# Performance work log

Hardware: AMD Instinct MI355X
Metric: run time of the kernel (lower is better)

## Reference

```python
import jax, jax.numpy as jnp
import numpy as np

B, S, N, DIN, DOUT = 8, 2048, 16, 1024, 1024

def setup_inputs() -> dict:
    key = jax.random.key(0)
    k1, k2, k3, k4 = jax.random.split(key, 4)
    x = jax.random.normal(k1, (B, S, DIN), dtype=jnp.float32)
    # selection_probs: per-batch mixture weights over total_options (rows sum to 1)
    logits = jax.random.uniform(k2, (B, N), dtype=jnp.float32)
    selection_probs = jax.nn.softmax(logits, axis=-1)
    # kaiming_uniform(a=sqrt(5)) over fan_in=DIN -> bound = 1/sqrt(DIN)
    bound = 1.0 / np.sqrt(DIN)
    weight = jax.random.uniform(k3, (N, DOUT, DIN), dtype=jnp.float32, minval=-bound, maxval=bound)
    bias = jax.random.uniform(k4, (N, DOUT), dtype=jnp.float32, minval=-bound, maxval=bound)
    return {"x": x, "selection_probs": selection_probs, "weight": weight, "bias": bias}

def reference(x, selection_probs, weight, bias):
    # Math identical to: einsum('nij,baj->bani', W, x) then einsum('bani,bn->bai', ., p)
    # but mixes weights per-batch first (same contraction, avoids the [B,S,N,DOUT] tensor).
    mixed_w = jnp.einsum('bn,nij->bij', selection_probs, weight)   # [B, DOUT, DIN]
    out = jnp.einsum('bij,baj->bai', mixed_w, x)                   # [B, S, DOUT]
    mixed_b = jnp.einsum('bn,ni->bi', selection_probs, bias)       # [B, DOUT]
    return out + mixed_b[:, None, :]
```

## Files before the change

### kernel.cpp

```cpp
#include <hip/hip_runtime.h>
#include <hip/hip_bf16.h>
#include <stdint.h>

#define BB 8
#define SS 2048
#define NEXP 16
#define DIN 1024
#define DOUT 1024

typedef short bf16x8 __attribute__((ext_vector_type(8)));
typedef float floatx4 __attribute__((ext_vector_type(4)));

__device__ __forceinline__ unsigned short f2bf(float f) {
    union { float f; unsigned int u; } v; v.f = f;
    unsigned int u = v.u;
    unsigned int r = u + 0x7FFFu + ((u >> 16) & 1u);
    return (unsigned short)(r >> 16);
}

__device__ __forceinline__ void gload16(const void* g, void* l) {
    __builtin_amdgcn_global_load_lds(
        (const __attribute__((address_space(1))) void*)g,
        (__attribute__((address_space(3))) void*)l,
        16, 0, 0);
}

__global__ __launch_bounds__(256) void prep_kernel(
    const float* __restrict__ x, const float* __restrict__ p,
    const float* __restrict__ w, const float* __restrict__ bias,
    unsigned short* __restrict__ xb, unsigned short* __restrict__ mw,
    float* __restrict__ mb)
{
    const int tid = threadIdx.x;
    const int blk = blockIdx.x;

    if (blk < 2048) {
        __shared__ float sp[BB * NEXP];
        if (tid < BB * NEXP) sp[tid] = p[tid];
        __syncthreads();
        const long t  = (long)blk * 256 + tid;
        const long j2 = t * 2;
        float acc[BB][2];
        #pragma unroll
        for (int b = 0; b < BB; ++b) { acc[b][0] = 0.f; acc[b][1] = 0.f; }
        #pragma unroll
        for (int n = 0; n < NEXP; ++n) {
            float2 wv = *(const float2*)(w + (long)n * DOUT * DIN + j2);
            #pragma unroll
            for (int b = 0; b < BB; ++b) {
                float pb = sp[b * NEXP + n];
                acc[b][0] += pb * wv.x; acc[b][1] += pb * wv.y;
            }
        }
        #pragma unroll
        for (int b = 0; b < BB; ++b) {
            unsigned o = (unsigned)f2bf(acc[b][0]) | ((unsigned)f2bf(acc[b][1]) << 16);
            *(unsigned*)(mw + (long)b * DOUT * DIN + j2) = o;
        }
    } else if (blk < 2080) {
        const long t = (long)(blk - 2048) * 256 + tid;
        const int b = (int)(t >> 10), i = (int)(t & 1023);
        float s = 0.f;
        #pragma unroll
        for (int n = 0; n < NEXP; ++n) s += p[b * NEXP + n] * bias[n * DOUT + i];
        mb[t] = s;
    } else {
        const int cb = blk - 2080;
        const float4* xv = (const float4*)x;
        uint2* xo = (uint2*)xb;
        const int base = cb * 1024 + tid;
        #pragma unroll
        for (int u = 0; u < 4; ++u) {
            float4 v = xv[base + u * 256];
            uint2 o;
            o.x = (unsigned)f2bf(v.x) | ((unsigned)f2bf(v.y) << 16);
            o.y = (unsigned)f2bf(v.z) | ((unsigned)f2bf(v.w) << 16);
            xo[base + u * 256] = o;
        }
    }
}

__global__ __launch_bounds__(256) void gemm_kernel(
    const unsigned short* __restrict__ xb,
    const unsigned short* __restrict__ mw,
    const float* __restrict__ mb,
    float* __restrict__ out)
{
    __shared__ __align__(16) unsigned short sA[128 * 64];
    __shared__ __align__(16) unsigned short sB[128 * 64];

    const int tid  = threadIdx.x;
    const int wave = tid >> 6;
    const int lane = tid & 63;
    const int b    = blockIdx.x;
    const int tileN = blockIdx.y * 128;
    const int tileM = blockIdx.z * 128;

    const unsigned short* Ag = xb + (long)b * SS * DIN;
    const unsigned short* Bg = mw + (long)b * DOUT * DIN;

    const int q     = lane >> 4;
    const int r16   = lane & 15;
    const int mBase = 64 * (wave >> 1);
    const int nBase = 64 * (wave & 1);

    const int sRow   = lane >> 3;
    const int sColSw = (((lane & 7) ^ sRow) * 8);

    const unsigned short* aSrc[4]; const unsigned short* bSrc[4];
    unsigned short* aDst[4]; unsigned short* bDst[4];
    #pragma unroll
    for (int c = 0; c < 4; ++c) {
        const int chunk = wave * 4 + c;
        const int row   = chunk * 8 + sRow;
        aSrc[c] = Ag + (long)(tileM + row) * DIN + sColSw;
        bSrc[c] = Bg + (long)(tileN + row) * DIN + sColSw;
        aDst[c] = &sA[chunk * 512];
        bDst[c] = &sB[chunk * 512];
    }

    const int swz  = r16 & 7;
    const int colK0 = ((q)     ^ swz) * 8;
    const int colK1 = ((q + 4) ^ swz) * 8;

    floatx4 acc[4][4];
    #pragma unroll
    for (int mi = 0; mi < 4; ++mi)
        #pragma unroll
        for (int ni = 0; ni < 4; ++ni)
            acc[mi][ni] = (floatx4){0.f, 0.f, 0.f, 0.f};

    #pragma unroll
    for (int t = 0; t < 16; ++t) {
        __syncthreads();
        #pragma unroll
        for (int c = 0; c < 4; ++c) {
            gload16(aSrc[c] + 64 * t, aDst[c]);
            gload16(bSrc[c] + 64 * t, bDst[c]);
        }
        __syncthreads();

        #pragma unroll
        for (int kh = 0; kh < 2; ++kh) {
            const int col = kh ? colK1 : colK0;
            bf16x8 af[4], bfv[4];
            #pragma unroll
            for (int i = 0; i < 4; ++i)
                af[i] = *(const bf16x8*)&sA[(mBase + 16 * i + r16) * 64 + col];
            #pragma unroll
            for (int i = 0; i < 4; ++i)
                bfv[i] = *(const bf16x8*)&sB[(nBase + 16 * i + r16) * 64 + col];
            #pragma unroll
            for (int mi = 0; mi < 4; ++mi)
                #pragma unroll
                for (int ni = 0; ni < 4; ++ni)
                    acc[mi][ni] = __builtin_amdgcn_mfma_f32_16x16x32_bf16(
                        af[mi], bfv[ni], acc[mi][ni], 0, 0, 0);
        }
    }

    float bv[4];
    #pragma unroll
    for (int ni = 0; ni < 4; ++ni)
        bv[ni] = mb[b * DOUT + tileN + nBase + 16 * ni + r16];

    #pragma unroll
    for (int mi = 0; mi < 4; ++mi) {
        #pragma unroll
        for (int rr = 0; rr < 4; ++rr) {
            const int row = tileM + mBase + 16 * mi + q * 4 + rr;
            float* orow = out + (long)b * SS * DOUT + (long)row * DOUT;
            #pragma unroll
            for (int ni = 0; ni < 4; ++ni)
                orow[tileN + nBase + 16 * ni + r16] = acc[mi][ni][rr] + bv[ni];
        }
    }
}

extern "C" void kernel_launch(void* const* d_in, const int* in_sizes, int n_in,
                              void* d_out, int out_size, void* d_ws, size_t ws_size,
                              hipStream_t stream) {
    const float* x    = (const float*)d_in[0];
    const float* p    = (const float*)d_in[1];
    const float* w    = (const float*)d_in[2];
    const float* bias = (const float*)d_in[3];
    float* out = (float*)d_out;

    unsigned short* xb = (unsigned short*)d_ws;
    unsigned short* mw = (unsigned short*)((char*)d_ws + (size_t)33554432);
    float*          mb = (float*)((char*)d_ws + (size_t)33554432 + 16777216);

    prep_kernel<<<dim3(6176), 256, 0, stream>>>(x, p, w, bias, xb, mw, mb);

    dim3 ggrid(BB, DOUT / 128, SS / 128);
    gemm_kernel<<<ggrid, 256, 0, stream>>>(xb, mw, mb, out);
}
```

Baseline: 209.2 us.

## Fuse fp32-to-bf16 conversion of x into the GEMM A-tile load

Removes the separate prep pass that converted x to bf16 in a workspace buffer. The GEMM now reads fp32 x directly, converts it to bf16 in registers and stores it to LDS using the same swizzled layout. The mixed-weight operand keeps its asynchronous global-to-LDS loads. This drops a full extra read and write of the activation tensor, but the GEMM now moves twice the bytes for the A operand on every tile reuse. It also swaps the async LDS loads for synchronous register loads, which may expose more latency in a loop that has no pipelining.

```diff
diff --git a/kernel.cpp b/kernel.cpp
--- a/kernel.cpp
+++ b/kernel.cpp
@@ -18,6 +18,12 @@
     return (unsigned short)(r >> 16);
 }
 
+__device__ __forceinline__ unsigned pk2(float a, float b) {
+    __hip_bfloat162 h = __float22bfloat162_rn(float2{a, b});
+    union { __hip_bfloat162 h; unsigned u; } cv; cv.h = h;
+    return cv.u;
+}
+
 __device__ __forceinline__ void gload16(const void* g, void* l) {
     __builtin_amdgcn_global_load_lds(
         (const __attribute__((address_space(1))) void*)g,
@@ -26,10 +32,9 @@
 }
 
 __global__ __launch_bounds__(256) void prep_kernel(
-    const float* __restrict__ x, const float* __restrict__ p,
-    const float* __restrict__ w, const float* __restrict__ bias,
-    unsigned short* __restrict__ xb, unsigned short* __restrict__ mw,
-    float* __restrict__ mb)
+    const float* __restrict__ p, const float* __restrict__ w,
+    const float* __restrict__ bias,
+    unsigned short* __restrict__ mw, float* __restrict__ mb)
 {
     const int tid = threadIdx.x;
     const int blk = blockIdx.x;
@@ -57,31 +62,18 @@
             unsigned o = (unsigned)f2bf(acc[b][0]) | ((unsigned)f2bf(acc[b][1]) << 16);
             *(unsigned*)(mw + (long)b * DOUT * DIN + j2) = o;
         }
-    } else if (blk < 2080) {
+    } else {
         const long t = (long)(blk - 2048) * 256 + tid;
         const int b = (int)(t >> 10), i = (int)(t & 1023);
         float s = 0.f;
         #pragma unroll
         for (int n = 0; n < NEXP; ++n) s += p[b * NEXP + n] * bias[n * DOUT + i];
         mb[t] = s;
-    } else {
-        const int cb = blk - 2080;
-        const float4* xv = (const float4*)x;
-        uint2* xo = (uint2*)xb;
-        const int base = cb * 1024 + tid;
-        #pragma unroll
-        for (int u = 0; u < 4; ++u) {
-            float4 v = xv[base + u * 256];
-            uint2 o;
-            o.x = (unsigned)f2bf(v.x) | ((unsigned)f2bf(v.y) << 16);
-            o.y = (unsigned)f2bf(v.z) | ((unsigned)f2bf(v.w) << 16);
-            xo[base + u * 256] = o;
-        }
     }
 }
 
 __global__ __launch_bounds__(256) void gemm_kernel(
-    const unsigned short* __restrict__ xb,
+    const float* __restrict__ x,
     const unsigned short* __restrict__ mw,
     const float* __restrict__ mb,
     float* __restrict__ out)
@@ -96,7 +88,7 @@
     const int tileN = blockIdx.y * 128;
     const int tileM = blockIdx.z * 128;
 
-    const unsigned short* Ag = xb + (long)b * SS * DIN;
+    const float*          Ag = x  + (long)b * SS * DIN;
     const unsigned short* Bg = mw + (long)b * DOUT * DIN;
 
     const int q     = lane >> 4;
@@ -107,7 +99,7 @@
     const int sRow   = lane >> 3;
     const int sColSw = (((lane & 7) ^ sRow) * 8);
 
-    const unsigned short* aSrc[4]; const unsigned short* bSrc[4];
+    const float* aSrc[4]; const unsigned short* bSrc[4];
     unsigned short* aDst[4]; unsigned short* bDst[4];
     #pragma unroll
     for (int c = 0; c < 4; ++c) {
@@ -115,7 +107,7 @@
         const int row   = chunk * 8 + sRow;
         aSrc[c] = Ag + (long)(tileM + row) * DIN + sColSw;
         bSrc[c] = Bg + (long)(tileN + row) * DIN + sColSw;
-        aDst[c] = &sA[chunk * 512];
+        aDst[c] = &sA[chunk * 512 + lane * 8];
         bDst[c] = &sB[chunk * 512];
     }
 
@@ -133,11 +125,21 @@
     #pragma unroll
     for (int t = 0; t < 16; ++t) {
         __syncthreads();
+
+        #pragma unroll
+        for (int c = 0; c < 4; ++c)
+            gload16(bSrc[c] + 64 * t, bDst[c]);
+
         #pragma unroll
         for (int c = 0; c < 4; ++c) {
-            gload16(aSrc[c] + 64 * t, aDst[c]);
-            gload16(bSrc[c] + 64 * t, bDst[c]);
+            float4 u = *(const float4*)(aSrc[c] + 64 * t);
+            float4 v = *(const float4*)(aSrc[c] + 64 * t + 4);
+            uint4 o;
+            o.x = pk2(u.x, u.y); o.y = pk2(u.z, u.w);
+            o.z = pk2(v.x, v.y); o.w = pk2(v.z, v.w);
+            *(uint4*)aDst[c] = o;
         }
+
         __syncthreads();
 
         #pragma unroll
@@ -186,12 +188,11 @@
     const float* bias = (const float*)d_in[3];
     float* out = (float*)d_out;
 
-    unsigned short* xb = (unsigned short*)d_ws;
-    unsigned short* mw = (unsigned short*)((char*)d_ws + (size_t)33554432);
-    float*          mb = (float*)((char*)d_ws + (size_t)33554432 + 16777216);
+    unsigned short* mw = (unsigned short*)d_ws;
+    float*          mb = (float*)((char*)d_ws + (size_t)16777216);
 
-    prep_kernel<<<dim3(6176), 256, 0, stream>>>(x, p, w, bias, xb, mw, mb);
+    prep_kernel<<<dim3(2080), 256, 0, stream>>>(p, w, bias, mw, mb);
 
     dim3 ggrid(BB, DOUT / 128, SS / 128);
-    gemm_kernel<<<ggrid, 256, 0, stream>>>(xb, mw, mb, out);
+    gemm_kernel<<<ggrid, 256, 0, stream>>>(x, mw, mb, out);
 }
```

Measured after the change: 247.1 us. +18.2%, slower.
